# Kernel tuning notes

Hardware: AMD Instinct MI355X
Metric: run time of the kernel (lower is better)

Reference implementation:

```python
import jax, jax.numpy as jnp
import numpy as np

RADIUS = 0.2
NSAMPLE = 32
USE_XYZ = True

B, N, S, C = 8, 8192, 2048, 64


def setup_inputs() -> dict:
    key = jax.random.key(0)
    k1, k2, k3 = jax.random.split(key, 3)
    xyz = jax.random.uniform(k1, (B, N, 3), dtype=jnp.float32)
    new_xyz = jax.random.uniform(k2, (B, S, 3), dtype=jnp.float32)
    features = jax.random.normal(k3, (B, N, C), dtype=jnp.float32)
    return {"xyz": xyz, "new_xyz": new_xyz, "features": features}


def _ball_query(new_xyz, xyz, radius, nsample):
    # new_xyz: (B,S,3), xyz: (B,N,3) -> idx (B,S,nsample) int32
    n = xyz.shape[1]
    d2 = jnp.sum((new_xyz[:, :, None, :] - xyz[:, None, :, :]) ** 2, axis=-1)  # (B,S,N)
    mask = d2 < radius * radius
    # keys: index j if inside ball else N (sentinel); smallest nsample keys = first
    # nsample in-ball indices in ascending j order (matches CUDA ball_query order).
    keys = jnp.where(mask, jnp.arange(n, dtype=jnp.int32), jnp.int32(n))
    neg_vals, _ = jax.lax.top_k(-keys, nsample)  # top_k of -keys -> smallest keys
    idx = -neg_vals  # (B,S,nsample), ascending
    first = idx[..., 0:1]
    idx = jnp.where(idx == n, first, idx)   # pad empty slots with first hit
    idx = jnp.where(idx == n, 0, idx)       # balls with zero hits -> index 0
    return idx


def _group(points, idx):
    # points: (B,N,D), idx: (B,S,K) -> (B,S,K,D)
    return jax.vmap(lambda p, i: p[i])(points, idx)


def reference(xyz, new_xyz, features):
    idx = _ball_query(new_xyz, xyz, RADIUS, NSAMPLE)
    grouped_xyz = _group(xyz, idx) - new_xyz[:, :, None, :]  # (B,S,K,3)
    grouped_feat = _group(features, idx)                      # (B,S,K,C)
    if USE_XYZ:
        new_features = jnp.concatenate([grouped_xyz, grouped_feat], axis=-1)
    else:
        new_features = grouped_feat
    return jnp.transpose(new_features, (0, 3, 1, 2))  # (B, C+3, S, K)
```

## Files before the change

### kernel.cpp

```cpp
#include <hip/hip_runtime.h>

#define BB 8
#define NN 8192
#define SS 2048
#define CC 64
#define NS 32
#define COUT 67
#define QT 4
#define SLOTS (QT*NS)
#define FSTR 65

typedef float f32x4 __attribute__((ext_vector_type(4)));

__global__ __launch_bounds__(256) void scan_kernel(
    const float* __restrict__ xyz,
    const float* __restrict__ new_xyz,
    int* __restrict__ idx_ws)
{
#pragma clang fp contract(off)
    const int wave = threadIdx.x >> 6;
    const int lane = threadIdx.x & 63;
    const int qid  = blockIdx.x * 4 + wave;
    const int b = qid >> 11;
    const int s = qid & 2047;

    const float R2 = 0.04f;

    const float* ctr = new_xyz + ((size_t)b * SS + s) * 3;
    const float cx = ctr[0], cy = ctr[1], cz = ctr[2];
    const float* xb = xyz + (size_t)b * NN * 3;

    int* myidx = idx_ws + (size_t)qid * NS;
    const unsigned long long lt = (1ull << lane) - 1ull;

    int total = 0;
    int firstIdx = -1;
    for (int j0 = 0; j0 < NN && total < NS; j0 += 256) {
        const float4* p4 = (const float4*)(xb + (size_t)(j0 + (lane << 2)) * 3);
        const float4 A  = p4[0];
        const float4 Bv = p4[1];
        const float4 Cv = p4[2];
        float d2v[4];
        {
            const float dx = A.x - cx, dy = A.y - cy, dz = A.z - cz;
            float d2 = dx * dx; d2 = d2 + dy * dy; d2 = d2 + dz * dz;
            d2v[0] = d2;
        }
        {
            const float dx = A.w - cx, dy = Bv.x - cy, dz = Bv.y - cz;
            float d2 = dx * dx; d2 = d2 + dy * dy; d2 = d2 + dz * dz;
            d2v[1] = d2;
        }
        {
            const float dx = Bv.z - cx, dy = Bv.w - cy, dz = Cv.x - cz;
            float d2 = dx * dx; d2 = d2 + dy * dy; d2 = d2 + dz * dz;
            d2v[2] = d2;
        }
        {
            const float dx = Cv.y - cx, dy = Cv.z - cy, dz = Cv.w - cz;
            float d2 = dx * dx; d2 = d2 + dy * dy; d2 = d2 + dz * dz;
            d2v[3] = d2;
        }

        unsigned long long M[4];
#pragma unroll
        for (int u = 0; u < 4; ++u) M[u] = __ballot(d2v[u] < R2);

        if (firstIdx < 0) {
            int fmin = 0x7fffffff;
#pragma unroll
            for (int u = 0; u < 4; ++u)
                if (M[u] != 0ull) {
                    const int j = j0 + (__builtin_ctzll(M[u]) << 2) + u;
                    fmin = (j < fmin) ? j : fmin;
                }
            if (fmin != 0x7fffffff) firstIdx = fmin;
        }

        int below = 0;
#pragma unroll
        for (int u = 0; u < 4; ++u) below += (int)__popcll(M[u] & lt);

        int own = 0;
#pragma unroll
        for (int u = 0; u < 4; ++u) {
            if (d2v[u] < R2) {
                const int pos = total + below + own;
                if (pos < NS) myidx[pos] = j0 + (lane << 2) + u;
                ++own;
            }
        }
#pragma unroll
        for (int u = 0; u < 4; ++u) total += (int)__popcll(M[u]);
    }
    if (total < NS) {
        const int fill = (total > 0) ? firstIdx : 0;
        if (lane >= total && lane < NS) myidx[lane] = fill;
    }
}

__global__ __launch_bounds__(256) void gather_kernel(
    const float* __restrict__ xyz,
    const float* __restrict__ new_xyz,
    const float* __restrict__ feat,
    const int* __restrict__ idx_ws,
    float* __restrict__ out)
{
#pragma clang fp contract(off)
    __shared__ float ft[SLOTS * FSTR];
    __shared__ float xt[3 * SLOTS];
    __shared__ int idx_sh[SLOTS];

    const int t   = threadIdx.x;
    const int bid = blockIdx.x;
    const int b     = bid & 7;
    const int sTile = bid >> 3;
    const int s0 = sTile * QT;
    const int qbase = (b << 11) + s0;

    if (t < SLOTS) idx_sh[t] = idx_ws[(size_t)qbase * NS + t];
    __syncthreads();

    if (t < SLOTS) {
        const int r = idx_sh[t];
        const int q = t >> 5;
        const float* ctr = new_xyz + ((size_t)b * SS + s0 + q) * 3;
        const float* p   = xyz + ((size_t)b * NN + r) * 3;
        xt[0 * SLOTS + t] = p[0] - ctr[0];
        xt[1 * SLOTS + t] = p[1] - ctr[1];
        xt[2 * SLOTS + t] = p[2] - ctr[2];
    }

    const int w  = t >> 6;
    const int ln = t & 63;
    const float* fb = feat + (size_t)b * NN * CC;
    for (int i = 0; i < 32; i += 4) {
        float v[4];
        int   mm[4];
#pragma unroll
        for (int u = 0; u < 4; ++u) {
            const int m = (w << 5) + i + u;
            mm[u] = m;
            v[u]  = fb[(size_t)idx_sh[m] * CC + ln];
        }
#pragma unroll
        for (int u = 0; u < 4; ++u)
            ft[mm[u] * FSTR + ln] = v[u];
    }
    __syncthreads();

    const size_t plane = (size_t)SS * NS;
    float* ob = out + ((size_t)b * COUT * SS + s0) * NS;
    for (int i = 0; i < 34; ++i) {
        const int tau = (i << 2) + w;
        if (tau < 134) {
            const int p  = tau >> 1;
            const int j  = tau & 1;
            const int sl = (j << 6) + ln;
            const float val = (p < 3) ? xt[p * SLOTS + sl]
                                      : ft[sl * FSTR + (p - 3)];
            __builtin_nontemporal_store(val, ob + (size_t)p * plane + sl);
        }
    }
}

extern "C" void kernel_launch(void* const* d_in, const int* in_sizes, int n_in,
                              void* d_out, int out_size, void* d_ws, size_t ws_size,
                              hipStream_t stream) {
    const float* xyz     = (const float*)d_in[0];
    const float* new_xyz = (const float*)d_in[1];
    const float* feat    = (const float*)d_in[2];
    float* out = (float*)d_out;
    int* idx_ws = (int*)d_ws;

    scan_kernel<<<dim3((BB * SS) / 4), dim3(256), 0, stream>>>(xyz, new_xyz, idx_ws);
    gather_kernel<<<dim3((BB * SS) / QT), dim3(256), 0, stream>>>(xyz, new_xyz, feat, idx_ws, out);
}
```

Before: 186.8 us.

## Fuse ball-query scan into gather kernel and use regular output stores

Merges the scan and gather kernels into one: each wave runs the ball query for one center and writes its indices straight into shared memory, so the global index workspace and the second launch go away. The output stores also change from nontemporal to plain stores. The cost is that each block now runs the scan before gathering, so its serial latency grows and the scan and gather phases can only overlap across different blocks.

```diff
diff --git a/kernel.cpp b/kernel.cpp
--- a/kernel.cpp
+++ b/kernel.cpp
@@ -10,100 +10,10 @@
 #define SLOTS (QT*NS)
 #define FSTR 65
 
-typedef float f32x4 __attribute__((ext_vector_type(4)));
-
-__global__ __launch_bounds__(256) void scan_kernel(
-    const float* __restrict__ xyz,
-    const float* __restrict__ new_xyz,
-    int* __restrict__ idx_ws)
-{
-#pragma clang fp contract(off)
-    const int wave = threadIdx.x >> 6;
-    const int lane = threadIdx.x & 63;
-    const int qid  = blockIdx.x * 4 + wave;
-    const int b = qid >> 11;
-    const int s = qid & 2047;
-
-    const float R2 = 0.04f;
-
-    const float* ctr = new_xyz + ((size_t)b * SS + s) * 3;
-    const float cx = ctr[0], cy = ctr[1], cz = ctr[2];
-    const float* xb = xyz + (size_t)b * NN * 3;
-
-    int* myidx = idx_ws + (size_t)qid * NS;
-    const unsigned long long lt = (1ull << lane) - 1ull;
-
-    int total = 0;
-    int firstIdx = -1;
-    for (int j0 = 0; j0 < NN && total < NS; j0 += 256) {
-        const float4* p4 = (const float4*)(xb + (size_t)(j0 + (lane << 2)) * 3);
-        const float4 A  = p4[0];
-        const float4 Bv = p4[1];
-        const float4 Cv = p4[2];
-        float d2v[4];
-        {
-            const float dx = A.x - cx, dy = A.y - cy, dz = A.z - cz;
-            float d2 = dx * dx; d2 = d2 + dy * dy; d2 = d2 + dz * dz;
-            d2v[0] = d2;
-        }
-        {
-            const float dx = A.w - cx, dy = Bv.x - cy, dz = Bv.y - cz;
-            float d2 = dx * dx; d2 = d2 + dy * dy; d2 = d2 + dz * dz;
-            d2v[1] = d2;
-        }
-        {
-            const float dx = Bv.z - cx, dy = Bv.w - cy, dz = Cv.x - cz;
-            float d2 = dx * dx; d2 = d2 + dy * dy; d2 = d2 + dz * dz;
-            d2v[2] = d2;
-        }
-        {
-            const float dx = Cv.y - cx, dy = Cv.z - cy, dz = Cv.w - cz;
-            float d2 = dx * dx; d2 = d2 + dy * dy; d2 = d2 + dz * dz;
-            d2v[3] = d2;
-        }
-
-        unsigned long long M[4];
-#pragma unroll
-        for (int u = 0; u < 4; ++u) M[u] = __ballot(d2v[u] < R2);
-
-        if (firstIdx < 0) {
-            int fmin = 0x7fffffff;
-#pragma unroll
-            for (int u = 0; u < 4; ++u)
-                if (M[u] != 0ull) {
-                    const int j = j0 + (__builtin_ctzll(M[u]) << 2) + u;
-                    fmin = (j < fmin) ? j : fmin;
-                }
-            if (fmin != 0x7fffffff) firstIdx = fmin;
-        }
-
-        int below = 0;
-#pragma unroll
-        for (int u = 0; u < 4; ++u) below += (int)__popcll(M[u] & lt);
-
-        int own = 0;
-#pragma unroll
-        for (int u = 0; u < 4; ++u) {
-            if (d2v[u] < R2) {
-                const int pos = total + below + own;
-                if (pos < NS) myidx[pos] = j0 + (lane << 2) + u;
-                ++own;
-            }
-        }
-#pragma unroll
-        for (int u = 0; u < 4; ++u) total += (int)__popcll(M[u]);
-    }
-    if (total < NS) {
-        const int fill = (total > 0) ? firstIdx : 0;
-        if (lane >= total && lane < NS) myidx[lane] = fill;
-    }
-}
-
-__global__ __launch_bounds__(256) void gather_kernel(
+__global__ __launch_bounds__(256) void fused_kernel(
     const float* __restrict__ xyz,
     const float* __restrict__ new_xyz,
     const float* __restrict__ feat,
-    const int* __restrict__ idx_ws,
     float* __restrict__ out)
 {
 #pragma clang fp contract(off)
@@ -112,13 +22,89 @@
     __shared__ int idx_sh[SLOTS];
 
     const int t   = threadIdx.x;
+    const int w   = t >> 6;
+    const int ln  = t & 63;
     const int bid = blockIdx.x;
     const int b     = bid & 7;
     const int sTile = bid >> 3;
     const int s0 = sTile * QT;
-    const int qbase = (b << 11) + s0;
 
-    if (t < SLOTS) idx_sh[t] = idx_ws[(size_t)qbase * NS + t];
+    {
+        const int s = s0 + w;
+        const float R2 = 0.04f;
+
+        const float* ctr = new_xyz + ((size_t)b * SS + s) * 3;
+        const float cx = ctr[0], cy = ctr[1], cz = ctr[2];
+        const float* xb = xyz + (size_t)b * NN * 3;
+
+        int* myidx = idx_sh + (w << 5);
+        const unsigned long long lt = (1ull << ln) - 1ull;
+
+        int total = 0;
+        int firstIdx = -1;
+        for (int j0 = 0; j0 < NN && total < NS; j0 += 256) {
+            const float4* p4 = (const float4*)(xb + (size_t)(j0 + (ln << 2)) * 3);
+            const float4 A  = p4[0];
+            const float4 Bv = p4[1];
+            const float4 Cv = p4[2];
+            float d2v[4];
+            {
+                const float dx = A.x - cx, dy = A.y - cy, dz = A.z - cz;
+                float d2 = dx * dx; d2 = d2 + dy * dy; d2 = d2 + dz * dz;
+                d2v[0] = d2;
+            }
+            {
+                const float dx = A.w - cx, dy = Bv.x - cy, dz = Bv.y - cz;
+                float d2 = dx * dx; d2 = d2 + dy * dy; d2 = d2 + dz * dz;
+                d2v[1] = d2;
+            }
+            {
+                const float dx = Bv.z - cx, dy = Bv.w - cy, dz = Cv.x - cz;
+                float d2 = dx * dx; d2 = d2 + dy * dy; d2 = d2 + dz * dz;
+                d2v[2] = d2;
+            }
+            {
+                const float dx = Cv.y - cx, dy = Cv.z - cy, dz = Cv.w - cz;
+                float d2 = dx * dx; d2 = d2 + dy * dy; d2 = d2 + dz * dz;
+                d2v[3] = d2;
+            }
+
+            unsigned long long M[4];
+#pragma unroll
+            for (int u = 0; u < 4; ++u) M[u] = __ballot(d2v[u] < R2);
+
+            if (firstIdx < 0) {
+                int fmin = 0x7fffffff;
+#pragma unroll
+                for (int u = 0; u < 4; ++u)
+                    if (M[u] != 0ull) {
+                        const int j = j0 + (__builtin_ctzll(M[u]) << 2) + u;
+                        fmin = (j < fmin) ? j : fmin;
+                    }
+                if (fmin != 0x7fffffff) firstIdx = fmin;
+            }
+
+            int below = 0;
+#pragma unroll
+            for (int u = 0; u < 4; ++u) below += (int)__popcll(M[u] & lt);
+
+            int own = 0;
+#pragma unroll
+            for (int u = 0; u < 4; ++u) {
+                if (d2v[u] < R2) {
+                    const int pos = total + below + own;
+                    if (pos < NS) myidx[pos] = j0 + (ln << 2) + u;
+                    ++own;
+                }
+            }
+#pragma unroll
+            for (int u = 0; u < 4; ++u) total += (int)__popcll(M[u]);
+        }
+        if (total < NS) {
+            const int fill = (total > 0) ? firstIdx : 0;
+            if (ln >= total && ln < NS) myidx[ln] = fill;
+        }
+    }
     __syncthreads();
 
     if (t < SLOTS) {
@@ -131,8 +117,6 @@
         xt[2 * SLOTS + t] = p[2] - ctr[2];
     }
 
-    const int w  = t >> 6;
-    const int ln = t & 63;
     const float* fb = feat + (size_t)b * NN * CC;
     for (int i = 0; i < 32; i += 4) {
         float v[4];
@@ -159,7 +143,7 @@
             const int sl = (j << 6) + ln;
             const float val = (p < 3) ? xt[p * SLOTS + sl]
                                       : ft[sl * FSTR + (p - 3)];
-            __builtin_nontemporal_store(val, ob + (size_t)p * plane + sl);
+            ob[(size_t)p * plane + sl] = val;
         }
     }
 }
@@ -171,8 +155,7 @@
     const float* new_xyz = (const float*)d_in[1];
     const float* feat    = (const float*)d_in[2];
     float* out = (float*)d_out;
-    int* idx_ws = (int*)d_ws;
+    (void)d_ws; (void)ws_size;
 
-    scan_kernel<<<dim3((BB * SS) / 4), dim3(256), 0, stream>>>(xyz, new_xyz, idx_ws);
-    gather_kernel<<<dim3((BB * SS) / QT), dim3(256), 0, stream>>>(xyz, new_xyz, feat, idx_ws, out);
+    fused_kernel<<<dim3((BB * SS) / QT), dim3(256), 0, stream>>>(xyz, new_xyz, feat, out);
 }
```

Result: faster. 179.1 us (-4.1%).
